# Kernel tuning notes

Hardware: AMD Instinct MI355X
Metric: run time of the kernel (lower is better)

## Reference

```python
import jax, jax.numpy as jnp
from jax import lax
import numpy as np

S = 2        # scale_factor
K = 5        # upsample_kernel_size
M = 64       # m_channels
C_IN = 128

def setup_inputs() -> dict:
    key = jax.random.key(0)
    k1, k2, k3, k4, k5 = jax.random.split(key, 5)
    B, C, H, W = 8, C_IN, 64, 64
    x = jax.random.normal(k1, (B, C, H, W), dtype=jnp.float32)
    compress_w = jax.random.normal(k2, (M, C, 1, 1), dtype=jnp.float32) * 0.05
    compress_b = jax.random.normal(k3, (M,), dtype=jnp.float32) * 0.05
    n_out = K * K * S * S  # 100
    encoder_w = jax.random.normal(k4, (n_out, M, 3, 3), dtype=jnp.float32) * 0.05
    encoder_b = jax.random.normal(k5, (n_out,), dtype=jnp.float32) * 0.05
    return {"x": x, "compress_w": compress_w, "compress_b": compress_b,
            "encoder_w": encoder_w, "encoder_b": encoder_b}

def _carafe(x, compress_w, compress_b, encoder_w, encoder_b):
    B, C, H, W = x.shape
    k, s = K, S
    nH, nW = s * H, s * W
    # 1x1 compress conv
    m = jnp.einsum('bchw,mc->bmhw', x, compress_w[:, :, 0, 0]) + compress_b[None, :, None, None]
    # 3x3 encoder conv, stride 1, pad 1 (SAME)
    ker = lax.conv_general_dilated(m, encoder_w, window_strides=(1, 1), padding='SAME',
                                   dimension_numbers=('NCHW', 'OIHW', 'NCHW'))
    ker = ker + encoder_b[None, :, None, None]  # (B, k*k*s*s, H, W)
    # PixelShuffle(s): (B, k*k, s, s, H, W) -> (B, k*k, H, s, W, s) -> (B, k*k, nH, nW)
    ker = ker.reshape(B, k * k, s, s, H, W).transpose(0, 1, 4, 2, 5, 3).reshape(B, k * k, nH, nW)
    ker = jax.nn.softmax(ker, axis=1)
    # Unfold(k, stride=1, pad=k//2): stack k*k shifted views, ordering (kh outer, kw inner)
    pad = k // 2
    xp = jnp.pad(x, ((0, 0), (0, 0), (pad, pad), (pad, pad)))
    patches = jnp.stack([xp[:, :, i:i + H, j:j + W] for i in range(k) for j in range(k)],
                        axis=2)  # (B, C, k*k, H, W)
    # nearest upsample by s on spatial dims
    up = jnp.repeat(jnp.repeat(patches, s, axis=3), s, axis=4)  # (B, C, k*k, nH, nW)
    # weighted local sum
    out = jnp.sum(up * ker[:, None, :, :, :], axis=2)  # (B, C, nH, nW)
    return out

def reference(x, compress_w, compress_b, encoder_w, encoder_b):
    return _carafe(x, compress_w, compress_b, encoder_w, encoder_b)
```

## Files before the change

kernel.cpp:

```cpp
#include <hip/hip_runtime.h>
#include <math.h>


typedef __attribute__((ext_vector_type(8))) short short8;
typedef __attribute__((ext_vector_type(4))) float floatx4;
typedef __attribute__((ext_vector_type(2))) float v2f;

__device__ __forceinline__ unsigned short f2bf(float f) {
  union { float f; unsigned int u; } v; v.f = f;
  unsigned int u = v.u + 0x7fffu + ((v.u >> 16) & 1u);
  return (unsigned short)(u >> 16);
}
__device__ __forceinline__ void unpack2(unsigned int u, float& lo, float& hi) {
  union { unsigned int u; float f; } a, b;
  a.u = u << 16; b.u = u & 0xffff0000u;
  lo = a.f; hi = b.f;
}
__device__ __forceinline__ v2f unpack2v(unsigned int u) {
  union { unsigned int u; float f; } a, b;
  a.u = u << 16; b.u = u & 0xffff0000u;
  return (v2f){a.f, b.f};
}

__global__ __launch_bounds__(256) void k_prep_pad(
    const float* __restrict__ x, const float* __restrict__ ew,
    const float* __restrict__ cw, unsigned short* __restrict__ a_prep,
    float* __restrict__ cwT, unsigned short* __restrict__ xpad) {
  const int blk = blockIdx.x;
  if (blk < 1024) {
    const float* xs = x + (size_t)blk * 4096;
    unsigned short* xd = xpad + (size_t)blk * 4896;
    for (int idx = threadIdx.x; idx < 1224; idx += 256) {
      int hp = idx / 18;
      int q = idx - hp * 18;
      int hh = hp - 2;
      int w0 = q * 4 - 2;
      float v0, v1, v2, v3;
      if (hh >= 0 && hh < 64 && w0 >= 0 && w0 + 3 < 64) {
        float4 xv = *(const float4*)&xs[hh * 64 + w0];
        v0 = xv.x; v1 = xv.y; v2 = xv.z; v3 = xv.w;
      } else {
        int base = hh * 64;
        bool hok = (hh >= 0 && hh < 64);
        v0 = (hok && w0 + 0 >= 0 && w0 + 0 < 64) ? xs[base + w0 + 0] : 0.f;
        v1 = (hok && w0 + 1 >= 0 && w0 + 1 < 64) ? xs[base + w0 + 1] : 0.f;
        v2 = (hok && w0 + 2 >= 0 && w0 + 2 < 64) ? xs[base + w0 + 2] : 0.f;
        v3 = (hok && w0 + 3 >= 0 && w0 + 3 < 64) ? xs[base + w0 + 3] : 0.f;
      }
      ushort4 o;
      o.x = f2bf(v0); o.y = f2bf(v1); o.z = f2bf(v2); o.w = f2bf(v3);
      *(ushort4*)&xd[idx * 4] = o;
    }
  } else {
    int idx = (blk - 1024) * 256 + (int)threadIdx.x;
    if (idx < 9 * 128 * 64) {
      int mo = idx & 63;
      int n = (idx >> 6) & 127;
      int tap = idx >> 13;
      float v = (n < 100) ? ew[(n * 64 + mo) * 9 + tap] : 0.f;
      a_prep[idx] = f2bf(v);
    } else {
      int r = idx - 9 * 128 * 64;
      int c = r >> 6, mo = r & 63;
      cwT[c * 64 + mo] = cw[mo * 128 + c];
    }
  }
}

__global__ __launch_bounds__(256) void k_compress(
    const float* __restrict__ x, const float* __restrict__ cwT,
    const float* __restrict__ cb, unsigned short* __restrict__ m_t) {
  __shared__ __align__(16) unsigned short ms[64][72];
  const int b = blockIdx.x >> 6;
  const int h = blockIdx.x & 63;
  const int wv = __builtin_amdgcn_readfirstlane((int)(threadIdx.x >> 6));
  const int lane = (int)(threadIdx.x & 63);
  const int mo0 = wv * 16;

  float acc[16];
#pragma unroll
  for (int k = 0; k < 16; ++k) acc[k] = 0.f;

  const float* xp = x + (((size_t)b * 128) * 64 + h) * 64 + lane;
  const float* wp = cwT + mo0;

#pragma unroll 4
  for (int c = 0; c < 128; ++c) {
    float xv = xp[(size_t)c * 4096];
#pragma unroll
    for (int k = 0; k < 16; ++k)
      acc[k] = fmaf(xv, wp[c * 64 + k], acc[k]);
  }

#pragma unroll
  for (int k = 0; k < 16; ++k) acc[k] += cb[mo0 + k];

#pragma unroll
  for (int k = 0; k < 8; ++k) {
    unsigned int p = ((unsigned int)f2bf(acc[2 * k + 1]) << 16) | f2bf(acc[2 * k]);
    *(unsigned int*)&ms[lane][mo0 + 2 * k] = p;
  }
  __syncthreads();
  const int t = threadIdx.x;
#pragma unroll
  for (int rep = 0; rep < 2; ++rep) {
    int idx = t + rep * 256;
    uint4 v = *(const uint4*)&ms[idx >> 3][(idx & 7) * 8];
    *(uint4*)&m_t[(size_t)blockIdx.x * 4096 + idx * 8] = v;
  }
}

__global__ __launch_bounds__(256) void k_encoder_softmax(
    const unsigned short* __restrict__ m_t, const unsigned short* __restrict__ a_prep,
    const float* __restrict__ eb, unsigned short* __restrict__ wgt_bf) {
  __shared__ __align__(16) float raw[128 * 66];
  unsigned short* m_s = (unsigned short*)raw;
  const int b = blockIdx.x >> 6;
  const int h = blockIdx.x & 63;
  const int t = threadIdx.x;

  for (int idx = t; idx < 3 * 64 * 8; idx += 256) {
    int r = idx >> 9;
    int rem = idx & 511;
    int w = rem >> 3, u = rem & 7;
    int hh = h + r - 1;
    uint4 val = make_uint4(0u, 0u, 0u, 0u);
    if (hh >= 0 && hh < 64)
      val = *(const uint4*)&m_t[(((b * 64 + hh) * 64 + w) * 64) + u * 8];
    *(uint4*)&m_s[(r * 64 + w) * 72 + u * 8] = val;
  }
  __syncthreads();

  const int wave = t >> 6, lane = t & 63;
  const int quad = lane >> 4, col = lane & 15;
  const int nbase = wave * 32;

  const floatx4 z4 = {0.f, 0.f, 0.f, 0.f};
  floatx4 acc[2][4];
#pragma unroll
  for (int i = 0; i < 2; ++i)
#pragma unroll
    for (int p = 0; p < 4; ++p) acc[i][p] = z4;

  const short8 z8 = {0, 0, 0, 0, 0, 0, 0, 0};

#pragma unroll
  for (int tap = 0; tap < 9; ++tap) {
    const int dh = tap / 3, dw = tap % 3;
#pragma unroll
    for (int half = 0; half < 2; ++half) {
      const int mo0 = half * 32;
      short8 a0 = *(const short8*)&a_prep[((tap * 128 + nbase + col) * 64) + mo0 + quad * 8];
      short8 a1 = *(const short8*)&a_prep[((tap * 128 + nbase + 16 + col) * 64) + mo0 + quad * 8];
#pragma unroll
      for (int p = 0; p < 4; ++p) {
        int wsrc = p * 16 + col + dw - 1;
        int wc = min(max(wsrc, 0), 63);
        short8 bf = *(const short8*)&m_s[(dh * 64 + wc) * 72 + mo0 + quad * 8];
        if (wsrc < 0 || wsrc > 63) bf = z8;
        acc[0][p] = __builtin_amdgcn_mfma_f32_16x16x32_bf16(a0, bf, acc[0][p], 0, 0, 0);
        acc[1][p] = __builtin_amdgcn_mfma_f32_16x16x32_bf16(a1, bf, acc[1][p], 0, 0, 0);
      }
    }
  }

  __syncthreads();
#pragma unroll
  for (int i = 0; i < 2; ++i)
#pragma unroll
    for (int p = 0; p < 4; ++p)
#pragma unroll
      for (int r = 0; r < 4; ++r)
        raw[(nbase + i * 16 + quad * 4 + r) * 66 + p * 16 + col] = acc[i][p][r];
  __syncthreads();

  const int q = wave;
  float v[25];
  float mx = -1e30f;
#pragma unroll
  for (int kk = 0; kk < 25; ++kk) {
    v[kk] = raw[(kk * 4 + q) * 66 + lane] + eb[kk * 4 + q];
    mx = fmaxf(mx, v[kk]);
  }
  float s = 0.f;
#pragma unroll
  for (int kk = 0; kk < 25; ++kk) {
    v[kk] = __expf(v[kk] - mx);
    s += v[kk];
  }
  float inv = 1.f / s;
  const int oh = 2 * h + (q >> 1);
  const int ow2 = 2 * lane + (q & 1);
#pragma unroll
  for (int kk = 0; kk < 25; ++kk)
    wgt_bf[((b * 25 + kk) * 128 + oh) * 128 + ow2] = f2bf(v[kk] * inv);
}

__global__ __launch_bounds__(256, 4) void k_reassemble(
    const unsigned short* __restrict__ xpad,
    const unsigned short* __restrict__ wgt_bf, float* __restrict__ out) {
  __shared__ __align__(16) unsigned short wgt_s[2][25][128];
  const int bh = blockIdx.x >> 1;
  const int chalf = blockIdx.x & 1;
  const int b = bh >> 6;
  const int h = bh & 63;
  const int t = threadIdx.x;

  for (int idx = t; idx < 800; idx += 256) {
    int r = (idx >= 400) ? 1 : 0;
    int rem = idx - r * 400;
    int kk = rem >> 4, ck = rem & 15;
    *(uint4*)&wgt_s[r][kk][ck * 8] =
        *(const uint4*)&wgt_bf[(((b * 25 + kk) * 128 + 2 * h + r) * 128) + ck * 8];
  }
  __syncthreads();

  const int wg = t & 15;
  const int cg = t >> 4;
  const int w0 = wg * 4;
  const int c0 = chalf * 64 + cg * 4;

  const unsigned short* xb =
      xpad + ((size_t)(b * 128 + c0) * 4896) + h * 72 + w0;

  v2f acc[2][4][4];
#pragma unroll
  for (int oh = 0; oh < 2; ++oh)
#pragma unroll
    for (int ch = 0; ch < 4; ++ch)
#pragma unroll
      for (int k = 0; k < 4; ++k) acc[oh][ch][k] = (v2f){0.f, 0.f};

  for (int i = 0; i < 5; ++i) {
    float xr[4][8];
#pragma unroll
    for (int ch = 0; ch < 4; ++ch) {
      uint4 rawv = *(const uint4*)(xb + ch * 4896 + i * 72);
      unpack2(rawv.x, xr[ch][0], xr[ch][1]);
      unpack2(rawv.y, xr[ch][2], xr[ch][3]);
      unpack2(rawv.z, xr[ch][4], xr[ch][5]);
      unpack2(rawv.w, xr[ch][6], xr[ch][7]);
    }
#pragma unroll
    for (int j = 0; j < 5; ++j) {
      const int ij = i * 5 + j;
#pragma unroll
      for (int oh = 0; oh < 2; ++oh) {
        uint4 wr = *(const uint4*)&wgt_s[oh][ij][w0 * 2];
        v2f wp[4];
        wp[0] = unpack2v(wr.x);
        wp[1] = unpack2v(wr.y);
        wp[2] = unpack2v(wr.z);
        wp[3] = unpack2v(wr.w);
#pragma unroll
        for (int k = 0; k < 4; ++k)
#pragma unroll
          for (int ch = 0; ch < 4; ++ch) {
            float xv = xr[ch][k + j];
            v2f xvv = {xv, xv};
            acc[oh][ch][k] += xvv * wp[k];
          }
      }
    }
  }

#pragma unroll
  for (int ch = 0; ch < 4; ++ch)
#pragma unroll
    for (int oh = 0; oh < 2; ++oh) {
      float* orow = out + ((size_t)(b * 128 + c0 + ch) * 128 + (2 * h + oh)) * 128 + w0 * 2;
      float4 f0 = make_float4(acc[oh][ch][0].x, acc[oh][ch][0].y,
                              acc[oh][ch][1].x, acc[oh][ch][1].y);
      float4 f1 = make_float4(acc[oh][ch][2].x, acc[oh][ch][2].y,
                              acc[oh][ch][3].x, acc[oh][ch][3].y);
      *(float4*)orow = f0;
      *(float4*)(orow + 4) = f1;
    }
}

extern "C" void kernel_launch(void* const* d_in, const int* in_sizes, int n_in,
                              void* d_out, int out_size, void* d_ws, size_t ws_size,
                              hipStream_t stream) {
  (void)in_sizes; (void)n_in; (void)out_size; (void)ws_size;
  const float* x  = (const float*)d_in[0];
  const float* cw = (const float*)d_in[1];
  const float* cb = (const float*)d_in[2];
  const float* ew = (const float*)d_in[3];
  const float* eb = (const float*)d_in[4];
  float* out = (float*)d_out;

  char* wsb = (char*)d_ws;
  unsigned short* m_t    = (unsigned short*)(wsb);
  unsigned short* a_prep = (unsigned short*)(wsb + 4194304);
  unsigned short* wgt_bf = (unsigned short*)(wsb + 4341760);
  unsigned short* xpad   = (unsigned short*)(wsb + 10895360);
  float*          cwT    = (float*)(wsb + 20922368);

  k_prep_pad<<<dim3(1344), dim3(256), 0, stream>>>(x, ew, cw, a_prep, cwT, xpad);
  k_compress<<<dim3(512), dim3(256), 0, stream>>>(x, cwT, cb, m_t);
  k_encoder_softmax<<<dim3(512), dim3(256), 0, stream>>>(m_t, a_prep, eb, wgt_bf);
  k_reassemble<<<dim3(1024), dim3(256), 0, stream>>>(xpad, wgt_bf, out);
}
```

Measured before the change: 156.7 us.

## Fuse encoder-softmax and reassembly into one kernel via shared memory

Merges the encoder/softmax kernel with the reassembly kernel. The softmax weights go to shared memory as bf16 instead of round-tripping through global memory, and each block then processes both channel halves in a loop. This removes the global write and read of the weight tensor and one kernel launch. The cost is half as many blocks, each doing more serial work, which can reduce occupancy and latency hiding.

```diff
diff --git a/kernel.cpp b/kernel.cpp
--- a/kernel.cpp
+++ b/kernel.cpp
@@ -110,11 +110,13 @@
   }
 }
 
-__global__ __launch_bounds__(256) void k_encoder_softmax(
+__global__ __launch_bounds__(256) void k_main(
     const unsigned short* __restrict__ m_t, const unsigned short* __restrict__ a_prep,
-    const float* __restrict__ eb, unsigned short* __restrict__ wgt_bf) {
+    const float* __restrict__ eb, const unsigned short* __restrict__ xpad,
+    float* __restrict__ out) {
   __shared__ __align__(16) float raw[128 * 66];
   unsigned short* m_s = (unsigned short*)raw;
+  unsigned short* wgt_s = (unsigned short*)raw;
   const int b = blockIdx.x >> 6;
   const int h = blockIdx.x & 63;
   const int t = threadIdx.x;
@@ -189,93 +191,81 @@
     s += v[kk];
   }
   float inv = 1.f / s;
-  const int oh = 2 * h + (q >> 1);
-  const int ow2 = 2 * lane + (q & 1);
-#pragma unroll
-  for (int kk = 0; kk < 25; ++kk)
-    wgt_bf[((b * 25 + kk) * 128 + oh) * 128 + ow2] = f2bf(v[kk] * inv);
-}
-
-__global__ __launch_bounds__(256, 4) void k_reassemble(
-    const unsigned short* __restrict__ xpad,
-    const unsigned short* __restrict__ wgt_bf, float* __restrict__ out) {
-  __shared__ __align__(16) unsigned short wgt_s[2][25][128];
-  const int bh = blockIdx.x >> 1;
-  const int chalf = blockIdx.x & 1;
-  const int b = bh >> 6;
-  const int h = bh & 63;
-  const int t = threadIdx.x;
-
-  for (int idx = t; idx < 800; idx += 256) {
-    int r = (idx >= 400) ? 1 : 0;
-    int rem = idx - r * 400;
-    int kk = rem >> 4, ck = rem & 15;
-    *(uint4*)&wgt_s[r][kk][ck * 8] =
-        *(const uint4*)&wgt_bf[(((b * 25 + kk) * 128 + 2 * h + r) * 128) + ck * 8];
+
+  __syncthreads();
+  {
+    const int ohl = q >> 1;
+    const int owp = 2 * lane + (q & 1);
+#pragma unroll
+    for (int kk = 0; kk < 25; ++kk)
+      wgt_s[(ohl * 25 + kk) * 128 + owp] = f2bf(v[kk] * inv);
   }
   __syncthreads();
 
   const int wg = t & 15;
   const int cg = t >> 4;
   const int w0 = wg * 4;
-  const int c0 = chalf * 64 + cg * 4;
-
-  const unsigned short* xb =
-      xpad + ((size_t)(b * 128 + c0) * 4896) + h * 72 + w0;
-
-  v2f acc[2][4][4];
-#pragma unroll
-  for (int oh = 0; oh < 2; ++oh)
+
+  for (int chalf = 0; chalf < 2; ++chalf) {
+    const int c0 = chalf * 64 + cg * 4;
+    const unsigned short* xb =
+        xpad + ((size_t)(b * 128 + c0) * 4896) + h * 72 + w0;
+
+    v2f accB[2][4][4];
+#pragma unroll
+    for (int oh = 0; oh < 2; ++oh)
+#pragma unroll
+      for (int ch = 0; ch < 4; ++ch)
+#pragma unroll
+        for (int k = 0; k < 4; ++k) accB[oh][ch][k] = (v2f){0.f, 0.f};
+
+    for (int i = 0; i < 5; ++i) {
+      float xr[4][8];
+#pragma unroll
+      for (int ch = 0; ch < 4; ++ch) {
+        uint4 rawv = *(const uint4*)(xb + ch * 4896 + i * 72);
+        unpack2(rawv.x, xr[ch][0], xr[ch][1]);
+        unpack2(rawv.y, xr[ch][2], xr[ch][3]);
+        unpack2(rawv.z, xr[ch][4], xr[ch][5]);
+        unpack2(rawv.w, xr[ch][6], xr[ch][7]);
+      }
+#pragma unroll
+      for (int j = 0; j < 5; ++j) {
+        const int ij = i * 5 + j;
+#pragma unroll
+        for (int oh = 0; oh < 2; ++oh) {
+          uint4 wr = *(const uint4*)&wgt_s[(oh * 25 + ij) * 128 + w0 * 2];
+          v2f wp[4];
+          wp[0] = unpack2v(wr.x);
+          wp[1] = unpack2v(wr.y);
+          wp[2] = unpack2v(wr.z);
+          wp[3] = unpack2v(wr.w);
+#pragma unroll
+          for (int k = 0; k < 4; ++k)
+#pragma unroll
+            for (int ch = 0; ch < 4; ++ch) {
+              float xv = xr[ch][k + j];
+              v2f xvv = {xv, xv};
+              accB[oh][ch][k] += xvv * wp[k];
+            }
+        }
+      }
+    }
+
 #pragma unroll
     for (int ch = 0; ch < 4; ++ch)
 #pragma unroll
-      for (int k = 0; k < 4; ++k) acc[oh][ch][k] = (v2f){0.f, 0.f};
-
-  for (int i = 0; i < 5; ++i) {
-    float xr[4][8];
-#pragma unroll
-    for (int ch = 0; ch < 4; ++ch) {
-      uint4 rawv = *(const uint4*)(xb + ch * 4896 + i * 72);
-      unpack2(rawv.x, xr[ch][0], xr[ch][1]);
-      unpack2(rawv.y, xr[ch][2], xr[ch][3]);
-      unpack2(rawv.z, xr[ch][4], xr[ch][5]);
-      unpack2(rawv.w, xr[ch][6], xr[ch][7]);
-    }
-#pragma unroll
-    for (int j = 0; j < 5; ++j) {
-      const int ij = i * 5 + j;
-#pragma unroll
       for (int oh = 0; oh < 2; ++oh) {
-        uint4 wr = *(const uint4*)&wgt_s[oh][ij][w0 * 2];
-        v2f wp[4];
-        wp[0] = unpack2v(wr.x);
-        wp[1] = unpack2v(wr.y);
-        wp[2] = unpack2v(wr.z);
-        wp[3] = unpack2v(wr.w);
-#pragma unroll
-        for (int k = 0; k < 4; ++k)
-#pragma unroll
-          for (int ch = 0; ch < 4; ++ch) {
-            float xv = xr[ch][k + j];
-            v2f xvv = {xv, xv};
-            acc[oh][ch][k] += xvv * wp[k];
-          }
-      }
-    }
-  }
-
-#pragma unroll
-  for (int ch = 0; ch < 4; ++ch)
-#pragma unroll
-    for (int oh = 0; oh < 2; ++oh) {
-      float* orow = out + ((size_t)(b * 128 + c0 + ch) * 128 + (2 * h + oh)) * 128 + w0 * 2;
-      float4 f0 = make_float4(acc[oh][ch][0].x, acc[oh][ch][0].y,
-                              acc[oh][ch][1].x, acc[oh][ch][1].y);
-      float4 f1 = make_float4(acc[oh][ch][2].x, acc[oh][ch][2].y,
-                              acc[oh][ch][3].x, acc[oh][ch][3].y);
-      *(float4*)orow = f0;
-      *(float4*)(orow + 4) = f1;
-    }
+        float* orow =
+            out + ((size_t)(b * 128 + c0 + ch) * 128 + (2 * h + oh)) * 128 + w0 * 2;
+        float4 f0 = make_float4(accB[oh][ch][0].x, accB[oh][ch][0].y,
+                                accB[oh][ch][1].x, accB[oh][ch][1].y);
+        float4 f1 = make_float4(accB[oh][ch][2].x, accB[oh][ch][2].y,
+                                accB[oh][ch][3].x, accB[oh][ch][3].y);
+        *(float4*)orow = f0;
+        *(float4*)(orow + 4) = f1;
+      }
+  }
 }
 
 extern "C" void kernel_launch(void* const* d_in, const int* in_sizes, int n_in,
@@ -292,12 +282,10 @@
   char* wsb = (char*)d_ws;
   unsigned short* m_t    = (unsigned short*)(wsb);
   unsigned short* a_prep = (unsigned short*)(wsb + 4194304);
-  unsigned short* wgt_bf = (unsigned short*)(wsb + 4341760);
-  unsigned short* xpad   = (unsigned short*)(wsb + 10895360);
-  float*          cwT    = (float*)(wsb + 20922368);
+  unsigned short* xpad   = (unsigned short*)(wsb + 4341760);
+  float*          cwT    = (float*)(wsb + 14368768);
 
   k_prep_pad<<<dim3(1344), dim3(256), 0, stream>>>(x, ew, cw, a_prep, cwT, xpad);
   k_compress<<<dim3(512), dim3(256), 0, stream>>>(x, cwT, cb, m_t);
-  k_encoder_softmax<<<dim3(512), dim3(256), 0, stream>>>(m_t, a_prep, eb, wgt_bf);
-  k_reassemble<<<dim3(1024), dim3(256), 0, stream>>>(xpad, wgt_bf, out);
-}
+  k_main<<<dim3(512), dim3(256), 0, stream>>>(m_t, a_prep, eb, xpad, out);
+}
```

New measurement: 145.4 us. 1.08x faster.
